# Kernel tuning notes

Hardware: AMD Instinct MI355X
Metric: run time of the kernel (lower is better)

The kernel has to match this reference:

```python
import jax, jax.numpy as jnp
import numpy as np

B, T, D, H = 2, 2048, 1024, 4
DK, DV = 1024, 2048          # key_dim = d_model*expand_k, value_dim = d_model*expand_v
HK, HV = DK // H, DV // H    # 256, 512 per-head dims
LR = 16                      # gate_low_rank_dim
EPS = 1e-5
GATE_NORM = 16.0             # gate_logit_normalizer


def _xavier(k, shape, gain):
    fan_in, fan_out = shape
    lim = gain * np.sqrt(6.0 / (fan_in + fan_out))
    return jax.random.uniform(k, shape, jnp.float32, -lim, lim)


def setup_inputs() -> dict:
    key = jax.random.key(0)
    ks = jax.random.split(key, 10)
    g_qkv = 2 ** (-2.5)
    return {
        "x": jax.random.normal(ks[0], (B, T, D), jnp.float32),
        "Wq": _xavier(ks[1], (D, DK), g_qkv),
        "Wk": _xavier(ks[2], (D, DK), g_qkv),
        "Wv": _xavier(ks[3], (D, DV), g_qkv),
        "Wg": _xavier(ks[4], (D, DV), g_qkv),
        "gk_w1": _xavier(ks[5], (D, LR), g_qkv),
        "gk_w2": _xavier(ks[6], (LR, DK), g_qkv),
        "gk_b": jnp.zeros((DK,), jnp.float32),
        "Wo": _xavier(ks[7], (DV, D), 2 ** (-1)),
        "rms_w": jnp.ones((HV,), jnp.float32),
    }


def _gla_scan(q, k, v, g):
    # q,k,g: [T, hk]; v: [T, hv]. Recurrence S_t = diag(exp(g_t)) S_{t-1} + k_t v_t^T; o_t = q_t @ S_t
    S0 = jnp.zeros((q.shape[-1], v.shape[-1]), q.dtype)

    def step(S, inp):
        qt, kt, vt, gt = inp
        S = jnp.exp(gt)[:, None] * S + kt[:, None] * vt[None, :]
        return S, qt @ S

    return jax.lax.scan(step, S0, (q, k, v, g))[1]  # [T, hv]


def _forward(x, Wq, Wk, Wv, Wg, gk_w1, gk_w2, gk_b, Wo, rms_w):
    b, t = x.shape[0], x.shape[1]
    scale = HK ** -0.5
    # projections -> [b, h, t, d_head]
    q = (x @ Wq).reshape(b, t, H, HK).transpose(0, 2, 1, 3) * scale
    k = (x @ Wk).reshape(b, t, H, HK).transpose(0, 2, 1, 3)
    v = (x @ Wv).reshape(b, t, H, HV).transpose(0, 2, 1, 3)
    # low-rank forget gate, log-space, fp32
    gl = (x @ gk_w1) @ gk_w2 + gk_b
    g = (jax.nn.log_sigmoid(gl.astype(jnp.float32)) / GATE_NORM)
    g = g.reshape(b, t, H, HK).transpose(0, 2, 1, 3)
    # per-(batch, head) linear-attention recurrence
    o = jax.vmap(jax.vmap(_gla_scan))(q, k, v, g)  # [b, h, t, hv]
    # group RMSNorm over head_v_dim
    o = o.transpose(0, 2, 1, 3)  # [b, t, h, hv]
    o = o * jax.lax.rsqrt(jnp.mean(o * o, axis=-1, keepdims=True) + EPS) * rms_w
    # output gate (swish) + out projection
    o = o.reshape(b, t, DV) * jax.nn.silu(x @ Wg)
    return o @ Wo  # [b, t, d_model]


def reference(x, Wq, Wk, Wv, Wg, gk_w1, gk_w2, gk_b, Wo, rms_w):
    return _forward(x, Wq, Wk, Wv, Wg, gk_w1, gk_w2, gk_b, Wo, rms_w)
```

## Files before the change

### kernel.cpp

```cpp
#include <hip/hip_runtime.h>
#include <cstdint>
#include <cstddef>


typedef unsigned short u16;
typedef __attribute__((ext_vector_type(8))) short s8v;
typedef __attribute__((ext_vector_type(4))) float f4v;

__device__ __forceinline__ u16 f2b(float f) {
  unsigned u = __builtin_bit_cast(unsigned, f);
  unsigned r = u + 0x7FFFu + ((u >> 16) & 1u);
  return (u16)(r >> 16);
}
__device__ __forceinline__ float b2f(u16 h) {
  unsigned u = ((unsigned)h) << 16;
  return __builtin_bit_cast(float, u);
}

__device__ __forceinline__ void cp16(const void* g, void* l) {
  __builtin_amdgcn_global_load_lds(
      (const __attribute__((address_space(1))) unsigned int*)g,
      (__attribute__((address_space(3))) unsigned int*)l, 16, 0, 0);
}

__device__ __forceinline__ void stage_tile(const u16* g, int ld, u16* lds,
                                           int wv, int ln) {
#pragma unroll
  for (int i = 0; i < 2; ++i) {
    const int c = wv * 2 + i;
    const u16* src = g + (size_t)(c * 16 + (ln >> 2)) * ld + (ln & 3) * 8;
    cp16(src, lds + c * 512);
  }
}

__device__ __forceinline__ void gemm_core(
    const u16* __restrict__ A, int lda, const u16* __restrict__ BT, int ldb,
    int K, u16* As, u16* Bs, f4v acc[4][4])
{
  const int tid = threadIdx.x;
  const int ln = tid & 63, wv = tid >> 6;
  const int wr = wv >> 1, wc = wv & 1;
  const int arow = wr * 64 + (ln & 15);
  const int brow = wc * 64 + (ln & 15);
  const int kq = (ln >> 4) * 8;
  stage_tile(A, lda, As, wv, ln);
  stage_tile(BT, ldb, Bs, wv, ln);
  __syncthreads();
  int cur = 0;
  for (int k0 = 0; k0 < K; k0 += 32) {
    const int nxt = cur ^ 1;
    if (k0 + 32 < K) {
      stage_tile(A + k0 + 32, lda, As + nxt * 4096, wv, ln);
      stage_tile(BT + k0 + 32, ldb, Bs + nxt * 4096, wv, ln);
    }
    const u16* Ab = As + cur * 4096;
    const u16* Bb = Bs + cur * 4096;
    s8v af[4], bf[4];
#pragma unroll
    for (int f = 0; f < 4; ++f)
      af[f] = *(const s8v*)(Ab + (arow + f * 16) * 32 + kq);
#pragma unroll
    for (int f = 0; f < 4; ++f)
      bf[f] = *(const s8v*)(Bb + (brow + f * 16) * 32 + kq);
#pragma unroll
    for (int mf = 0; mf < 4; ++mf)
#pragma unroll
      for (int nf = 0; nf < 4; ++nf)
        acc[mf][nf] = __builtin_amdgcn_mfma_f32_16x16x32_bf16(
            af[mf], bf[nf], acc[mf][nf], 0, 0, 0);
    __syncthreads();
    cur = nxt;
  }
}

#define EPI_SETUP                                            \
  const int tid = threadIdx.x;                               \
  const int ln = tid & 63, wv = tid >> 6;                    \
  const int wr = wv >> 1, wc = wv & 1;

#define ZERO_ACC(acc)                                        \
  _Pragma("unroll")                                          \
  for (int zi = 0; zi < 4; ++zi)                             \
    _Pragma("unroll")                                        \
    for (int zj = 0; zj < 4; ++zj)                           \
      acc[zi][zj] = (f4v){0.f, 0.f, 0.f, 0.f};

__global__ __launch_bounds__(256) void cast_b(const float* __restrict__ in,
                                              u16* __restrict__ out) {
  const int i = blockIdx.x * 256 + threadIdx.x;
  const float4 v = ((const float4*)in)[i];
  u16* p = out + i * 4;
  p[0] = f2b(v.x); p[1] = f2b(v.y); p[2] = f2b(v.z); p[3] = f2b(v.w);
}

__global__ __launch_bounds__(256) void wtrans(const float* __restrict__ in,
                                              u16* __restrict__ out, int R, int C) {
  __shared__ float t[32][33];
  const int c0 = blockIdx.x * 32, r0 = blockIdx.y * 32;
  const int lx = threadIdx.x & 31, ly = threadIdx.x >> 5;
#pragma unroll
  for (int i = 0; i < 32; i += 8)
    t[ly + i][lx] = in[(size_t)(r0 + ly + i) * C + c0 + lx];
  __syncthreads();
#pragma unroll
  for (int i = 0; i < 32; i += 8)
    out[(size_t)(c0 + ly + i) * R + r0 + lx] = f2b(t[lx][ly + i]);
}

__global__ __launch_bounds__(256) void trans_b16(const u16* __restrict__ in,
                                                 u16* __restrict__ out, int R, int C) {
  __shared__ u16 t[32][33];
  const size_t boff = (size_t)blockIdx.z * R * C;
  const int c0 = blockIdx.x * 32, r0 = blockIdx.y * 32;
  const int lx = threadIdx.x & 31, ly = threadIdx.x >> 5;
#pragma unroll
  for (int i = 0; i < 32; i += 8)
    t[ly + i][lx] = in[boff + (size_t)(r0 + ly + i) * C + c0 + lx];
  __syncthreads();
#pragma unroll
  for (int i = 0; i < 32; i += 8)
    out[boff + (size_t)(c0 + ly + i) * R + r0 + lx] = t[lx][ly + i];
}

__global__ __launch_bounds__(256) void lowrank1(
    const float* __restrict__ x, const float* __restrict__ w1,
    float* __restrict__ tmp)
{
  const int idx = blockIdx.x * 256 + threadIdx.x;
  const int m = idx >> 4, i = idx & 15;
  const float* xr = x + (size_t)m * 1024;
  float acc = 0.f;
#pragma unroll 4
  for (int kk = 0; kk < 1024; kk += 4) {
    const float4 xv = *(const float4*)(xr + kk);
    acc = fmaf(xv.x, w1[(kk + 0) * 16 + i], acc);
    acc = fmaf(xv.y, w1[(kk + 1) * 16 + i], acc);
    acc = fmaf(xv.z, w1[(kk + 2) * 16 + i], acc);
    acc = fmaf(xv.w, w1[(kk + 3) * 16 + i], acc);
  }
  tmp[idx] = acc;
}

__global__ __launch_bounds__(256) void gate_cum(
    const float* __restrict__ tmp, const float* __restrict__ w2,
    const float* __restrict__ bias, u16* __restrict__ dq, u16* __restrict__ dk,
    float* __restrict__ Dc)
{
  __shared__ float ls_t[2048];
  const int b = blockIdx.y >> 4, c = blockIdx.y & 15;
  const int h = blockIdx.x;
  const int i = threadIdx.x;
  const int n = h * 256 + i;
  const int bh = b * 4 + h;
  const float* tp = tmp + ((size_t)(b * 2048 + c * 128)) * 16;
#pragma unroll
  for (int r = 0; r < 8; ++r) ls_t[r * 256 + threadIdx.x] = tp[r * 256 + threadIdx.x];
  __syncthreads();
  float w2c[16];
#pragma unroll
  for (int r = 0; r < 16; ++r) w2c[r] = w2[r * 1024 + n];
  const float bn = bias[n];
  const size_t base = ((size_t)bh * 2048 + c * 128) * 256 + i;
  float B = 0.f;
  for (int t = 0; t < 128; ++t) {
    float gl = bn;
    const float* tr = ls_t + t * 16;
#pragma unroll
    for (int r = 0; r < 16; ++r) gl = fmaf(tr[r], w2c[r], gl);
    const float ls = fminf(gl, 0.f) - log1pf(expf(-fabsf(gl)));
    B += ls * 0.0625f;
    const float eB = expf(B);
    dq[base + (size_t)t * 256] = f2b(eB);
    dk[base + (size_t)t * 256] = f2b(1.f / eB);
  }
  Dc[(bh * 16 + c) * 256 + i] = expf(B);
}

__global__ __launch_bounds__(256) void proj_all(
    const u16* __restrict__ xb, const u16* __restrict__ WT,
    const u16* __restrict__ dq, const u16* __restrict__ dk,
    u16* __restrict__ qt, u16* __restrict__ kt,
    u16* __restrict__ vr, u16* __restrict__ gpre)
{
  __shared__ __align__(16) u16 As[8192], Bs[8192];
  const int id = blockIdx.x;
  const int wg = (id & 7) * 192 + (id >> 3);
  const int m0 = (wg & 31) * 128, n0 = (wg >> 5) * 128;
  f4v acc[4][4];
  ZERO_ACC(acc)
  gemm_core(xb + (size_t)m0 * 1024, 1024, WT + (size_t)n0 * 1024, 1024, 1024,
            As, Bs, acc);
  EPI_SETUP
#pragma unroll
  for (int mf = 0; mf < 4; ++mf)
#pragma unroll
    for (int nf = 0; nf < 4; ++nf)
#pragma unroll
      for (int r = 0; r < 4; ++r) {
        const int m = m0 + wr * 64 + mf * 16 + ((ln >> 4) << 2) + r;
        const int n = n0 + wc * 64 + nf * 16 + (ln & 15);
        const float val = acc[mf][nf][r];
        const int b = m >> 11, t = m & 2047;
        if (n0 < 1024) {
          const int bh = b * 4 + (n >> 8), i = n & 255;
          const size_t off = ((size_t)bh * 2048 + t) * 256 + i;
          qt[off] = f2b(val * 0.0625f * b2f(dq[off]));
        } else if (n0 < 2048) {
          const int nn = n - 1024;
          const int bh = b * 4 + (nn >> 8), i = nn & 255;
          const size_t off = ((size_t)bh * 2048 + t) * 256 + i;
          kt[off] = f2b(val * b2f(dk[off]));
        } else if (n0 < 4096) {
          const int nn = n - 2048;
          const int bh = b * 4 + (nn >> 9), j = nn & 511;
          vr[((size_t)bh * 2048 + t) * 512 + j] = f2b(val);
        } else {
          gpre[(size_t)m * 2048 + (n - 4096)] = f2b(val);
        }
      }
}

__global__ __launch_bounds__(256) void scan_gemms(
    const u16* __restrict__ vT, const u16* __restrict__ ktT,
    const u16* __restrict__ qt, const u16* __restrict__ kt,
    u16* __restrict__ UT, u16* __restrict__ Aw)
{
  __shared__ __align__(16) u16 As[8192], Bs[8192];
  const int bhc = blockIdx.y, bh = bhc >> 4, c = bhc & 15;
  f4v acc[4][4];
  ZERO_ACC(acc)
  if (blockIdx.x < 8) {
    const int mt = blockIdx.x >> 1, nt = blockIdx.x & 1;
    gemm_core(vT + ((size_t)bh * 512 + mt * 128) * 2048 + c * 128, 2048,
              ktT + ((size_t)bh * 256 + nt * 128) * 2048 + c * 128, 2048, 128,
              As, Bs, acc);
    EPI_SETUP
#pragma unroll
    for (int mf = 0; mf < 4; ++mf)
#pragma unroll
      for (int nf = 0; nf < 4; ++nf)
#pragma unroll
        for (int r = 0; r < 4; ++r) {
          const int j = mt * 128 + wr * 64 + mf * 16 + ((ln >> 4) << 2) + r;
          const int i = nt * 128 + wc * 64 + nf * 16 + (ln & 15);
          UT[(((size_t)(bh * 512 + j)) * 16 + c) * 256 + i] = f2b(acc[mf][nf][r]);
        }
  } else {
    const size_t base = ((size_t)bh * 2048 + c * 128) * 256;
    gemm_core(qt + base, 256, kt + base, 256, 256, As, Bs, acc);
    EPI_SETUP
    u16* Ap = Aw + (size_t)bhc * 16384;
#pragma unroll
    for (int mf = 0; mf < 4; ++mf)
#pragma unroll
      for (int nf = 0; nf < 4; ++nf)
#pragma unroll
        for (int r = 0; r < 4; ++r) {
          const int t = wr * 64 + mf * 16 + ((ln >> 4) << 2) + r;
          const int s = wc * 64 + nf * 16 + (ln & 15);
          Ap[t * 128 + s] = (s <= t) ? f2b(acc[mf][nf][r]) : (u16)0;
        }
  }
}

__global__ __launch_bounds__(256) void state_scan(
    u16* __restrict__ UT, const float* __restrict__ Dc)
{
  const int blk = blockIdx.x;
  const int bh = blk >> 9, j = blk & 511;
  const int i = threadIdx.x;
  u16* Up = UT + ((size_t)(bh * 512 + j)) * 16 * 256 + i;
  const float* Dp = Dc + bh * 16 * 256 + i;
  float S = 0.f;
  for (int c = 0; c < 16; ++c) {
    const float u = b2f(Up[c * 256]);
    Up[c * 256] = f2b(S);
    S = Dp[c * 256] * (S + u);
  }
}

__global__ __launch_bounds__(256) void intra_k(
    const u16* __restrict__ Aw, const u16* __restrict__ qt,
    const u16* __restrict__ vT, const u16* __restrict__ UT, u16* __restrict__ ob)
{
  __shared__ __align__(16) u16 As[8192], Bs[8192];
  const int jt = blockIdx.x;
  const int bhc = blockIdx.y, bh = bhc >> 4, c = bhc & 15;
  f4v acc[4][4];
  ZERO_ACC(acc)
  gemm_core(Aw + (size_t)bhc * 16384, 128,
            vT + ((size_t)bh * 512 + jt * 128) * 2048 + c * 128, 2048, 128,
            As, Bs, acc);
  gemm_core(qt + ((size_t)bh * 2048 + c * 128) * 256, 256,
            UT + ((size_t)(bh * 512 + jt * 128)) * 4096 + (size_t)c * 256, 4096, 256,
            As, Bs, acc);
  EPI_SETUP
  const int b = bh >> 2, h = bh & 3;
#pragma unroll
  for (int mf = 0; mf < 4; ++mf)
#pragma unroll
    for (int nf = 0; nf < 4; ++nf)
#pragma unroll
      for (int r = 0; r < 4; ++r) {
        const int t = c * 128 + wr * 64 + mf * 16 + ((ln >> 4) << 2) + r;
        const int j = jt * 128 + wc * 64 + nf * 16 + (ln & 15);
        ob[((size_t)(b * 2048 + t)) * 2048 + h * 512 + j] = f2b(acc[mf][nf][r]);
      }
}

__global__ __launch_bounds__(256) void rms_silu(
    u16* __restrict__ o, const u16* __restrict__ gpre, const float* __restrict__ w)
{
  const int grp = blockIdx.x * 4 + (threadIdx.x >> 6);
  const int lane = threadIdx.x & 63;
  const size_t base = (size_t)(grp >> 2) * 2048 + (grp & 3) * 512;
  float xv[8];
  float ss = 0.f;
#pragma unroll
  for (int i = 0; i < 8; ++i) {
    xv[i] = b2f(o[base + i * 64 + lane]);
    ss = fmaf(xv[i], xv[i], ss);
  }
#pragma unroll
  for (int off = 1; off < 64; off <<= 1) ss += __shfl_xor(ss, off, 64);
  const float r = rsqrtf(ss * (1.f / 512.f) + 1e-5f);
#pragma unroll
  for (int i = 0; i < 8; ++i) {
    const int cidx = i * 64 + lane;
    const float gp = b2f(gpre[base + cidx]);
    const float sig = 1.f / (1.f + expf(-gp));
    o[base + cidx] = f2b(xv[i] * r * w[cidx] * gp * sig);
  }
}

__global__ __launch_bounds__(256) void gemm_out(
    const u16* __restrict__ ob, const u16* __restrict__ WoT,
    float* __restrict__ pout)
{
  __shared__ __align__(16) u16 As[8192], Bs[8192];
  const int id = blockIdx.x;
  const int wg = (id & 7) * 64 + (id >> 3);
  const int ks = wg >> 8;
  const int tt = wg & 255;
  const int m0 = (tt & 31) * 128, n0 = (tt >> 5) * 128;
  f4v acc[4][4];
  ZERO_ACC(acc)
  gemm_core(ob + (size_t)m0 * 2048 + ks * 1024, 2048,
            WoT + (size_t)n0 * 2048 + ks * 1024, 2048, 1024, As, Bs, acc);
  EPI_SETUP
  float* po = pout + (size_t)ks * 4194304;
#pragma unroll
  for (int mf = 0; mf < 4; ++mf)
#pragma unroll
    for (int nf = 0; nf < 4; ++nf)
#pragma unroll
      for (int r = 0; r < 4; ++r) {
        const int m = m0 + wr * 64 + mf * 16 + ((ln >> 4) << 2) + r;
        const int n = n0 + wc * 64 + nf * 16 + (ln & 15);
        po[(size_t)m * 1024 + n] = acc[mf][nf][r];
      }
}

__global__ __launch_bounds__(256) void reduce_out(
    const float* __restrict__ p, float* __restrict__ out)
{
  const int i = blockIdx.x * 256 + threadIdx.x;
  const float4 a = ((const float4*)p)[i];
  const float4 b = ((const float4*)(p + 4194304))[i];
  ((float4*)out)[i] = make_float4(a.x + b.x, a.y + b.y, a.z + b.z, a.w + b.w);
}

extern "C" void kernel_launch(void* const* d_in, const int* in_sizes, int n_in,
                              void* d_out, int out_size, void* d_ws, size_t ws_size,
                              hipStream_t stream) {
  const float* x    = (const float*)d_in[0];
  const float* Wq   = (const float*)d_in[1];
  const float* Wk   = (const float*)d_in[2];
  const float* Wv   = (const float*)d_in[3];
  const float* Wg   = (const float*)d_in[4];
  const float* w1   = (const float*)d_in[5];
  const float* w2   = (const float*)d_in[6];
  const float* gb   = (const float*)d_in[7];
  const float* Wo   = (const float*)d_in[8];
  const float* rmsw = (const float*)d_in[9];
  float* out = (float*)d_out;

  char* W = (char*)d_ws;
  u16*   xb   = (u16*)W;   W += (size_t)8  << 20;
  u16*   WTa  = (u16*)W;   W += (size_t)12 << 20;
  u16*   WoT  = (u16*)W;   W += (size_t)4  << 20;
  u16*   qt   = (u16*)W;   W += (size_t)8  << 20;
  u16*   kt   = (u16*)W;   W += (size_t)8  << 20;
  u16*   vr   = (u16*)W;   W += (size_t)16 << 20;
  u16*   vT   = (u16*)W;   W += (size_t)16 << 20;
  u16*   ktT  = (u16*)W;   W += (size_t)8  << 20;
  u16*   gpre = (u16*)W;   W += (size_t)16 << 20;
  float* tmp  = (float*)W; W += (size_t)256 << 10;
  float* Dc   = (float*)W; W += (size_t)128 << 10;
  u16*   dq   = (u16*)W;   W += (size_t)8  << 20;
  u16*   dk   = (u16*)W;   W += (size_t)8  << 20;
  u16*   UT   = (u16*)W;   W += (size_t)32 << 20;
  u16*   Aw   = (u16*)W;   W += (size_t)4  << 20;
  u16*   ob   = (u16*)W;   W += (size_t)16 << 20;
  float* pout = (float*)W; W += (size_t)32 << 20;

  hipLaunchKernelGGL(lowrank1, dim3(256), dim3(256), 0, stream, x, w1, tmp);
  hipLaunchKernelGGL(gate_cum, dim3(4, 32), dim3(256), 0, stream,
                     tmp, w2, gb, dq, dk, Dc);

  hipLaunchKernelGGL(cast_b, dim3(4096), dim3(256), 0, stream, x, xb);
  hipLaunchKernelGGL(wtrans, dim3(32, 32), dim3(256), 0, stream, Wq, WTa, 1024, 1024);
  hipLaunchKernelGGL(wtrans, dim3(32, 32), dim3(256), 0, stream, Wk, WTa + 1048576, 1024, 1024);
  hipLaunchKernelGGL(wtrans, dim3(64, 32), dim3(256), 0, stream, Wv, WTa + 2097152, 1024, 2048);
  hipLaunchKernelGGL(wtrans, dim3(64, 32), dim3(256), 0, stream, Wg, WTa + 4194304, 1024, 2048);
  hipLaunchKernelGGL(wtrans, dim3(32, 64), dim3(256), 0, stream, Wo, WoT, 2048, 1024);

  hipLaunchKernelGGL(proj_all, dim3(1536), dim3(256), 0, stream,
                     xb, WTa, dq, dk, qt, kt, vr, gpre);

  hipLaunchKernelGGL(trans_b16, dim3(8, 64, 8), dim3(256), 0, stream,
                     kt, ktT, 2048, 256);
  hipLaunchKernelGGL(trans_b16, dim3(16, 64, 8), dim3(256), 0, stream,
                     vr, vT, 2048, 512);

  hipLaunchKernelGGL(scan_gemms, dim3(9, 128), dim3(256), 0, stream,
                     vT, ktT, qt, kt, UT, Aw);
  hipLaunchKernelGGL(state_scan, dim3(4096), dim3(256), 0, stream, UT, Dc);
  hipLaunchKernelGGL(intra_k, dim3(4, 128), dim3(256), 0, stream, Aw, qt, vT, UT, ob);

  hipLaunchKernelGGL(rms_silu, dim3(4096), dim3(256), 0, stream, ob, gpre, rmsw);
  hipLaunchKernelGGL(gemm_out, dim3(512), dim3(256), 0, stream, ob, WoT, pout);
  hipLaunchKernelGGL(reduce_out, dim3(4096), dim3(256), 0, stream, pout, out);
}
```

Baseline: 321.9 us.

## Triple-buffer GEMM core with vmcnt waits and remap proj_all tiles per XCD

Replaces the double-buffered LDS pipeline in the shared GEMM core with a three-slot ring that prefetches two k-steps ahead. Each step waits on explicit vmcnt counts instead of a full __syncthreads drain, so more global-to-LDS loads stay in flight. LDS buffers in all GEMM kernels grow by half to hold the third slot, which may lower occupancy. proj_all also reassigns tiles so each XCD owns a contiguous range of N columns, aiming at better L2 reuse of the weight tiles.

```diff
diff --git a/kernel.cpp b/kernel.cpp
--- a/kernel.cpp
+++ b/kernel.cpp
@@ -39,22 +39,26 @@
 {
   const int tid = threadIdx.x;
   const int ln = tid & 63, wv = tid >> 6;
-  const int wr = wv >> 1, wc = wv & 1;
-  const int arow = wr * 64 + (ln & 15);
-  const int brow = wc * 64 + (ln & 15);
+  const int arow = (wv >> 1) * 64 + (ln & 15);
+  const int brow = (wv & 1) * 64 + (ln & 15);
   const int kq = (ln >> 4) * 8;
+  const int nt = K >> 5;
   stage_tile(A, lda, As, wv, ln);
   stage_tile(BT, ldb, Bs, wv, ln);
-  __syncthreads();
-  int cur = 0;
-  for (int k0 = 0; k0 < K; k0 += 32) {
-    const int nxt = cur ^ 1;
-    if (k0 + 32 < K) {
-      stage_tile(A + k0 + 32, lda, As + nxt * 4096, wv, ln);
-      stage_tile(BT + k0 + 32, ldb, Bs + nxt * 4096, wv, ln);
-    }
-    const u16* Ab = As + cur * 4096;
-    const u16* Bb = Bs + cur * 4096;
+  stage_tile(A + 32, lda, As + 4096, wv, ln);
+  stage_tile(BT + 32, ldb, Bs + 4096, wv, ln);
+  stage_tile(A + 64, lda, As + 8192, wv, ln);
+  stage_tile(BT + 64, ldb, Bs + 8192, wv, ln);
+  int slot = 0;
+  for (int t = 0; t < nt; ++t) {
+    const int rem = nt - 1 - t;
+    if (rem >= 2)      asm volatile("s_waitcnt vmcnt(8)" ::: "memory");
+    else if (rem == 1) asm volatile("s_waitcnt vmcnt(4)" ::: "memory");
+    else               asm volatile("s_waitcnt vmcnt(0)" ::: "memory");
+    __builtin_amdgcn_s_barrier();
+    __builtin_amdgcn_sched_barrier(0);
+    const u16* Ab = As + slot * 4096;
+    const u16* Bb = Bs + slot * 4096;
     s8v af[4], bf[4];
 #pragma unroll
     for (int f = 0; f < 4; ++f)
@@ -68,8 +72,13 @@
       for (int nf = 0; nf < 4; ++nf)
         acc[mf][nf] = __builtin_amdgcn_mfma_f32_16x16x32_bf16(
             af[mf], bf[nf], acc[mf][nf], 0, 0, 0);
-    __syncthreads();
-    cur = nxt;
+    __builtin_amdgcn_sched_barrier(0);
+    __builtin_amdgcn_s_barrier();
+    if (t + 3 < nt) {
+      stage_tile(A + (t + 3) * 32, lda, As + slot * 4096, wv, ln);
+      stage_tile(BT + (t + 3) * 32, ldb, Bs + slot * 4096, wv, ln);
+    }
+    slot = (slot == 2) ? 0 : slot + 1;
   }
 }
 
@@ -182,10 +191,11 @@
     u16* __restrict__ qt, u16* __restrict__ kt,
     u16* __restrict__ vr, u16* __restrict__ gpre)
 {
-  __shared__ __align__(16) u16 As[8192], Bs[8192];
+  __shared__ __align__(16) u16 As[12288], Bs[12288];
   const int id = blockIdx.x;
-  const int wg = (id & 7) * 192 + (id >> 3);
-  const int m0 = (wg & 31) * 128, n0 = (wg >> 5) * 128;
+  const int xcd = id & 7, j = id >> 3;
+  const int m0 = (j / 6) * 128;
+  const int n0 = (xcd * 6 + (j % 6)) * 128;
   f4v acc[4][4];
   ZERO_ACC(acc)
   gemm_core(xb + (size_t)m0 * 1024, 1024, WT + (size_t)n0 * 1024, 1024, 1024,
@@ -212,8 +222,8 @@
           kt[off] = f2b(val * b2f(dk[off]));
         } else if (n0 < 4096) {
           const int nn = n - 2048;
-          const int bh = b * 4 + (nn >> 9), j = nn & 511;
-          vr[((size_t)bh * 2048 + t) * 512 + j] = f2b(val);
+          const int bh = b * 4 + (nn >> 9), jj = nn & 511;
+          vr[((size_t)bh * 2048 + t) * 512 + jj] = f2b(val);
         } else {
           gpre[(size_t)m * 2048 + (n - 4096)] = f2b(val);
         }
@@ -225,7 +235,7 @@
     const u16* __restrict__ qt, const u16* __restrict__ kt,
     u16* __restrict__ UT, u16* __restrict__ Aw)
 {
-  __shared__ __align__(16) u16 As[8192], Bs[8192];
+  __shared__ __align__(16) u16 As[12288], Bs[12288];
   const int bhc = blockIdx.y, bh = bhc >> 4, c = bhc & 15;
   f4v acc[4][4];
   ZERO_ACC(acc)
@@ -283,7 +293,7 @@
     const u16* __restrict__ Aw, const u16* __restrict__ qt,
     const u16* __restrict__ vT, const u16* __restrict__ UT, u16* __restrict__ ob)
 {
-  __shared__ __align__(16) u16 As[8192], Bs[8192];
+  __shared__ __align__(16) u16 As[12288], Bs[12288];
   const int jt = blockIdx.x;
   const int bhc = blockIdx.y, bh = bhc >> 4, c = bhc & 15;
   f4v acc[4][4];
@@ -337,7 +347,7 @@
     const u16* __restrict__ ob, const u16* __restrict__ WoT,
     float* __restrict__ pout)
 {
-  __shared__ __align__(16) u16 As[8192], Bs[8192];
+  __shared__ __align__(16) u16 As[12288], Bs[12288];
   const int id = blockIdx.x;
   const int wg = (id & 7) * 64 + (id >> 3);
   const int ks = wg >> 8;
```

New measurement: 317.6 us. About the same (-1.4%).
